# Kernel optimization log

Measured on AMD Instinct MI355X. Metric: run time of the kernel, lower is better.

Reference implementation:

```python
import jax, jax.numpy as jnp
import numpy as np

M_FACTORS = [8, 8, 8, 8]
N_FACTORS = [8, 8, 8, 8]
RANK = 8
E = 8
B = 8
SEQ = 512
M_IN = int(np.prod(M_FACTORS))   # 4096
N_OUT = int(np.prod(N_FACTORS))  # 4096


def setup_inputs() -> dict:
    key = jax.random.key(0)
    k1, k2, k3, k4, k5 = jax.random.split(key, 5)
    X = jax.random.normal(k1, (B, SEQ, M_IN), dtype=jnp.float32)
    gates = jax.random.uniform(k2, (B, E), dtype=jnp.float32)
    # TT cores: [E, r_i, factor, r_{i+1}]; boundary ranks are 1.
    core_first = jax.random.normal(k3, (E, 1, M_FACTORS[0], RANK), dtype=jnp.float32)
    cores_mid = jax.random.normal(k4, (6, E, RANK, 8, RANK), dtype=jnp.float32)
    core_last = jax.random.normal(k5, (E, RANK, N_FACTORS[-1], 1), dtype=jnp.float32)
    return {"X": X, "gates": gates, "core_first": core_first,
            "cores_mid": cores_mid, "core_last": core_last}


def _tt_forward(X, gates, core_first, cores_mid, core_last):
    b, s, _ = X.shape
    # View X as [B, 1, seq, m_k-1, ..., m_0] (m factors reversed), rank dim = 1.
    tt = X.reshape((b, s) + tuple(M_FACTORS[::-1]))[:, None]
    cores = [core_first] + [cores_mid[i] for i in range(cores_mid.shape[0])] + [core_last]
    num_m = len(M_FACTORS)
    # Input-factor contractions: 'b r ... m, b r m p -> b p ...'
    for i in range(num_m):
        merged = jnp.einsum('be,ermp->brmp', gates, cores[i])  # [B, r, m_f, p]
        tt = jnp.einsum('br...m,brmp->bp...', tt, merged)
    # Output-factor expansions: 'b r ..., b r n p -> b p ... n'
    for i in range(len(N_FACTORS)):
        merged = jnp.einsum('be,ernp->brnp', gates, cores[num_m + i])  # [B, r, n_f, p]
        tt = jnp.einsum('br...,brnp->bp...n', tt, merged)
    return tt.reshape(b, s, -1)  # [B, seq, prod(n_factors)]


def reference(X, gates, core_first, cores_mid, core_last):
    return _tt_forward(X, gates, core_first, cores_mid, core_last)
```

## Files before the change

### kernel.cpp

```cpp
#include <hip/hip_runtime.h>


#define MC_ 8

__global__ __launch_bounds__(256) void k_compose(
    const float* __restrict__ gates,
    const float* __restrict__ core_first,
    const float* __restrict__ cores_mid,
    const float* __restrict__ core_last,
    float* __restrict__ Kin,
    float* __restrict__ Kout)
{
  const int part = blockIdx.x;
  const int b    = blockIdx.y;
  const int t    = threadIdx.x;

  __shared__ float g[8];
  __shared__ float mg[3200];
  __shared__ __align__(16) float A2[512];
  __shared__ __align__(16) float A3[4096];
  __shared__ __align__(16) float C2[512];
  __shared__ __align__(16) float C3[4096];

  if (t < 8) g[t] = gates[b*8 + t];
  __syncthreads();

  for (int idx = t; idx < 3200; idx += 256) {
    float acc = 0.f;
    if (idx < 64) {
      #pragma unroll
      for (int e = 0; e < 8; ++e) acc += g[e] * core_first[e*64 + idx];
    } else if (idx < 3136) {
      const int i = (idx - 64) >> 9;
      const int w = (idx - 64) & 511;
      #pragma unroll
      for (int e = 0; e < 8; ++e) acc += g[e] * cores_mid[(i*8 + e)*512 + w];
    } else {
      const int w = idx - 3136;
      #pragma unroll
      for (int e = 0; e < 8; ++e) acc += g[e] * core_last[e*64 + w];
    }
    mg[idx] = acc;
  }
  __syncthreads();

  const float* mg0 = mg;
  const float* mg1 = mg + 64;
  const float* mg2 = mg + 64 + 512;
  const float* mg3 = mg + 64 + 1024;
  const float* mg4 = mg + 64 + 1536;
  const float* mg5 = mg + 64 + 2048;
  const float* mg6 = mg + 64 + 2560;
  const float* mg7 = mg + 3136;

  for (int idx = t; idx < 1024; idx += 256) {
    if (idx < 512) {
      const int mm = idx >> 3, p2 = idx & 7;
      const int m1 = mm >> 3, m0 = mm & 7;
      float acc = 0.f;
      #pragma unroll
      for (int p1 = 0; p1 < 8; ++p1)
        acc += mg0[m0*8 + p1] * mg1[p1*64 + m1*8 + p2];
      A2[idx] = acc;
    } else {
      const int id = idx - 512;
      const int p6 = id >> 6, n2 = (id >> 3) & 7, n3 = id & 7;
      float acc = 0.f;
      #pragma unroll
      for (int p7 = 0; p7 < 8; ++p7)
        acc += mg6[p6*64 + n2*8 + p7] * mg7[p7*8 + n3];
      C2[id] = acc;
    }
  }
  __syncthreads();

  for (int idx = t; idx < 8192; idx += 256) {
    if (idx < 4096) {
      const int rest = idx >> 3, p3 = idx & 7;
      const int m2 = rest >> 6, mm = rest & 63;
      float acc = 0.f;
      #pragma unroll
      for (int p2 = 0; p2 < 8; ++p2)
        acc += A2[mm*8 + p2] * mg2[p2*64 + m2*8 + p3];
      A3[idx] = acc;
    } else {
      const int id = idx - 4096;
      const int p5 = id >> 9, n1 = (id >> 6) & 7, nn = id & 63;
      float acc = 0.f;
      #pragma unroll
      for (int p6 = 0; p6 < 8; ++p6)
        acc += mg5[p5*64 + n1*8 + p6] * C2[p6*64 + nn];
      C3[id] = acc;
    }
  }
  __syncthreads();

  {
    float* kb = Kin + b*32768 + part*4096;
    #pragma unroll
    for (int rr = 0; rr < 2; ++rr) {
      const int r = t*2 + rr;
      #pragma unroll
      for (int p4 = 0; p4 < 8; ++p4) {
        float acc = 0.f;
        #pragma unroll
        for (int p3 = 0; p3 < 8; ++p3)
          acc += A3[r*8 + p3] * mg3[p3*64 + part*8 + p4];
        kb[r*8 + p4] = acc;
      }
    }
    float* ob = Kout + b*32768 + part*512;
    #pragma unroll
    for (int jj = 0; jj < 2; ++jj) {
      const int j = t*2 + jj;
      #pragma unroll
      for (int p4 = 0; p4 < 8; ++p4) {
        float acc = 0.f;
        #pragma unroll
        for (int p5 = 0; p5 < 8; ++p5)
          acc += mg4[p4*64 + part*8 + p5] * C3[p5*512 + j];
        ob[p4*4096 + j] = acc;
      }
    }
  }
}

#define XPAD 516

__global__ __launch_bounds__(256) void k_vpart(
    const float* __restrict__ X,
    const float* __restrict__ Kin,
    float* __restrict__ Vpart)
{
  const int stile = blockIdx.x;
  const int mc    = blockIdx.y;
  const int b     = blockIdx.z;
  const int t     = threadIdx.x;

  __shared__ __align__(16) float xs[16 * XPAD];
  __shared__ __align__(16) float lkT[8 * XPAD];
  __shared__ float vred[2 * 16 * 8];

  {
    const float* xbase = X + ((size_t)(b*512 + stile*16) * 4096) + mc*512;
    #pragma unroll
    for (int i = 0; i < 8; ++i) {
      const int idx = t + i*256;
      const int r = idx >> 7;
      const int c = idx & 127;
      const float4 v = ((const float4*)(xbase + (size_t)r*4096))[c];
      *(float4*)&xs[r*XPAD + c*4] = v;
    }
  }
  {
    const float4* kb = (const float4*)(Kin + b*32768 + mc*4096);
    #pragma unroll
    for (int i = 0; i < 4; ++i) {
      const int idx = t + i*256;
      const int m  = idx >> 1;
      const int ph = (idx & 1) * 4;
      const float4 v = kb[idx];
      lkT[(ph+0)*XPAD + m] = v.x;
      lkT[(ph+1)*XPAD + m] = v.y;
      lkT[(ph+2)*XPAD + m] = v.z;
      lkT[(ph+3)*XPAD + m] = v.w;
    }
  }
  __syncthreads();

  {
    const int h  = t >> 7;
    const int sp = t & 127;
    const int sl = sp >> 3;
    const int p  = sp & 7;
    const float* xrow = &xs[sl*XPAD + h*256];
    const float* krow = &lkT[p*XPAD + h*256];
    float acc = 0.f;
    #pragma unroll 8
    for (int j = 0; j < 64; ++j) {
      const float4 a = *(const float4*)(xrow + j*4);
      const float4 k = *(const float4*)(krow + j*4);
      acc += a.x*k.x + a.y*k.y + a.z*k.z + a.w*k.w;
    }
    vred[t] = acc;
  }
  __syncthreads();

  if (t < 128) {
    const float v = vred[t] + vred[128 + t];
    Vpart[((size_t)(b*MC_ + mc)*512 + stile*16)*8 + t] = v;
  }
}

__global__ __launch_bounds__(256) void k_out(
    const float* __restrict__ Vpart,
    const float* __restrict__ Kout,
    float* __restrict__ Out)
{
  const int nc = blockIdx.x;
  const int sg = blockIdx.y;
  const int b  = blockIdx.z;
  const int t  = threadIdx.x;

  __shared__ __align__(16) float vs[32*8];

  {
    const float* vp = Vpart + ((size_t)b*MC_*512 + sg*32)*8 + t;
    float a = 0.f;
    #pragma unroll
    for (int mc = 0; mc < MC_; ++mc) a += vp[(size_t)mc*512*8];
    vs[t] = a;
  }

  float4 kr[8];
  {
    const float* kb = Kout + b*32768 + nc*1024 + t*4;
    #pragma unroll
    for (int p = 0; p < 8; ++p) kr[p] = *(const float4*)(kb + p*4096);
  }
  __syncthreads();

  float* ob = Out + (size_t)(b*512 + sg*32)*4096 + nc*1024 + t*4;
  for (int s = 0; s < 32; ++s) {
    const float* vv = &vs[s*8];
    float o0 = 0.f, o1 = 0.f, o2 = 0.f, o3 = 0.f;
    #pragma unroll
    for (int p = 0; p < 8; ++p) {
      const float v = vv[p];
      o0 += v * kr[p].x; o1 += v * kr[p].y; o2 += v * kr[p].z; o3 += v * kr[p].w;
    }
    *(float4*)(ob + (size_t)s*4096) = make_float4(o0, o1, o2, o3);
  }
}

extern "C" void kernel_launch(void* const* d_in, const int* in_sizes, int n_in,
                              void* d_out, int out_size, void* d_ws, size_t ws_size,
                              hipStream_t stream) {
  const float* X     = (const float*)d_in[0];
  const float* gates = (const float*)d_in[1];
  const float* cf    = (const float*)d_in[2];
  const float* cm    = (const float*)d_in[3];
  const float* cl    = (const float*)d_in[4];
  float* out = (float*)d_out;

  float* ws    = (float*)d_ws;
  float* Kin   = ws;
  float* Kout  = ws + 262144;
  float* Vpart = ws + 524288;

  k_compose<<<dim3(8, 8),          256, 0, stream>>>(gates, cf, cm, cl, Kin, Kout);
  k_vpart <<<dim3(32, MC_, 8),     256, 0, stream>>>(X, Kin, Vpart);
  k_out   <<<dim3(4, 16, 8),       256, 0, stream>>>(Vpart, Kout, out);
}
```

Before: 137.2 us.

## Fuse input projection and output expansion into one kernel with transposed Kin

Merges the X·Kin reduction and the V·Kout expansion into a single kernel, so the Vpart intermediate and one launch go away. Each block now covers 8 sequence rows across all of M, streaming transposed Kin chunks through shared memory with register prefetch and reducing with wave shuffles. The compose kernel writes Kin transposed and pads A3 to avoid shared-memory bank conflicts. The cost is a smaller grid (512 blocks), higher register use, and each block re-reading the full per-batch Kin and Kout.

```diff
diff --git a/kernel.cpp b/kernel.cpp
--- a/kernel.cpp
+++ b/kernel.cpp
@@ -1,14 +1,12 @@
 #include <hip/hip_runtime.h>
 
-
-#define MC_ 8
 
 __global__ __launch_bounds__(256) void k_compose(
     const float* __restrict__ gates,
     const float* __restrict__ core_first,
     const float* __restrict__ cores_mid,
     const float* __restrict__ core_last,
-    float* __restrict__ Kin,
+    float* __restrict__ KinT,
     float* __restrict__ Kout)
 {
   const int part = blockIdx.x;
@@ -18,7 +16,7 @@
   __shared__ float g[8];
   __shared__ float mg[3200];
   __shared__ __align__(16) float A2[512];
-  __shared__ __align__(16) float A3[4096];
+  __shared__ __align__(16) float A3[512 * 9];
   __shared__ __align__(16) float C2[512];
   __shared__ __align__(16) float C3[4096];
 
@@ -82,7 +80,7 @@
       #pragma unroll
       for (int p2 = 0; p2 < 8; ++p2)
         acc += A2[mm*8 + p2] * mg2[p2*64 + m2*8 + p3];
-      A3[idx] = acc;
+      A3[rest*9 + p3] = acc;
     } else {
       const int id = idx - 4096;
       const int p5 = id >> 9, n1 = (id >> 6) & 7, nn = id & 63;
@@ -96,23 +94,23 @@
   __syncthreads();
 
   {
-    float* kb = Kin + b*32768 + part*4096;
+    float* kb = KinT + b*32768;
     #pragma unroll
     for (int rr = 0; rr < 2; ++rr) {
-      const int r = t*2 + rr;
+      const int r = rr*256 + t;
       #pragma unroll
       for (int p4 = 0; p4 < 8; ++p4) {
         float acc = 0.f;
         #pragma unroll
         for (int p3 = 0; p3 < 8; ++p3)
-          acc += A3[r*8 + p3] * mg3[p3*64 + part*8 + p4];
-        kb[r*8 + p4] = acc;
+          acc += A3[r*9 + p3] * mg3[p3*64 + part*8 + p4];
+        kb[p4*4096 + part*512 + r] = acc;
       }
     }
     float* ob = Kout + b*32768 + part*512;
     #pragma unroll
     for (int jj = 0; jj < 2; ++jj) {
-      const int j = t*2 + jj;
+      const int j = jj*256 + t;
       #pragma unroll
       for (int p4 = 0; p4 < 8; ++p4) {
         float acc = 0.f;
@@ -125,111 +123,124 @@
   }
 }
 
-#define XPAD 516
-
-__global__ __launch_bounds__(256) void k_vpart(
+__global__ __launch_bounds__(256, 2) void k_fused(
     const float* __restrict__ X,
-    const float* __restrict__ Kin,
-    float* __restrict__ Vpart)
-{
-  const int stile = blockIdx.x;
-  const int mc    = blockIdx.y;
-  const int b     = blockIdx.z;
-  const int t     = threadIdx.x;
-
-  __shared__ __align__(16) float xs[16 * XPAD];
-  __shared__ __align__(16) float lkT[8 * XPAD];
-  __shared__ float vred[2 * 16 * 8];
-
-  {
-    const float* xbase = X + ((size_t)(b*512 + stile*16) * 4096) + mc*512;
-    #pragma unroll
-    for (int i = 0; i < 8; ++i) {
-      const int idx = t + i*256;
-      const int r = idx >> 7;
-      const int c = idx & 127;
-      const float4 v = ((const float4*)(xbase + (size_t)r*4096))[c];
-      *(float4*)&xs[r*XPAD + c*4] = v;
-    }
-  }
-  {
-    const float4* kb = (const float4*)(Kin + b*32768 + mc*4096);
-    #pragma unroll
-    for (int i = 0; i < 4; ++i) {
-      const int idx = t + i*256;
-      const int m  = idx >> 1;
-      const int ph = (idx & 1) * 4;
-      const float4 v = kb[idx];
-      lkT[(ph+0)*XPAD + m] = v.x;
-      lkT[(ph+1)*XPAD + m] = v.y;
-      lkT[(ph+2)*XPAD + m] = v.z;
-      lkT[(ph+3)*XPAD + m] = v.w;
-    }
-  }
-  __syncthreads();
-
-  {
-    const int h  = t >> 7;
-    const int sp = t & 127;
-    const int sl = sp >> 3;
-    const int p  = sp & 7;
-    const float* xrow = &xs[sl*XPAD + h*256];
-    const float* krow = &lkT[p*XPAD + h*256];
-    float acc = 0.f;
-    #pragma unroll 8
-    for (int j = 0; j < 64; ++j) {
-      const float4 a = *(const float4*)(xrow + j*4);
-      const float4 k = *(const float4*)(krow + j*4);
-      acc += a.x*k.x + a.y*k.y + a.z*k.z + a.w*k.w;
-    }
-    vred[t] = acc;
-  }
-  __syncthreads();
-
-  if (t < 128) {
-    const float v = vred[t] + vred[128 + t];
-    Vpart[((size_t)(b*MC_ + mc)*512 + stile*16)*8 + t] = v;
-  }
-}
-
-__global__ __launch_bounds__(256) void k_out(
-    const float* __restrict__ Vpart,
+    const float* __restrict__ KinT,
     const float* __restrict__ Kout,
     float* __restrict__ Out)
 {
-  const int nc = blockIdx.x;
-  const int sg = blockIdx.y;
-  const int b  = blockIdx.z;
-  const int t  = threadIdx.x;
-
-  __shared__ __align__(16) float vs[32*8];
+  const int stile = blockIdx.x;
+  const int b     = blockIdx.y;
+  const int t     = threadIdx.x;
+  const int lane  = t & 63;
+  const int sp    = t >> 6;
+
+  __shared__ __align__(16) float lkT[8 * 1024];
+  __shared__ __align__(16) float vs[8 * 8];
+
+  const int s0 = stile * 8;
+
+  const float* ksrc = KinT + (size_t)b*32768 + t*4;
+  float*       kdst = lkT + t*4;
+  float4 R[8];
+
+  float4 acc[2][8];
+  #pragma unroll
+  for (int s2 = 0; s2 < 2; ++s2)
+    #pragma unroll
+    for (int p = 0; p < 8; ++p) acc[s2][p] = make_float4(0.f, 0.f, 0.f, 0.f);
+
+  const float* xb = X + ((size_t)(b*512 + s0 + sp*2)) * 4096 + lane*4;
+
+  #pragma unroll
+  for (int i = 0; i < 8; ++i) R[i] = *(const float4*)(ksrc + i*4096);
+  #pragma unroll
+  for (int i = 0; i < 8; ++i) *(float4*)(kdst + i*1024) = R[i];
+  __syncthreads();
+
+  #pragma unroll
+  for (int mc = 0; mc < 4; ++mc) {
+    if (mc < 3) {
+      #pragma unroll
+      for (int i = 0; i < 8; ++i)
+        R[i] = *(const float4*)(ksrc + i*4096 + (mc + 1)*1024);
+    }
+    #pragma unroll
+    for (int j = 0; j < 4; ++j) {
+      const float4 x0 = *(const float4*)(xb + (mc*256 + j*64)*4);
+      const float4 x1 = *(const float4*)(xb + 4096 + (mc*256 + j*64)*4);
+      #pragma unroll
+      for (int p = 0; p < 8; ++p) {
+        const float4 k = *(const float4*)(lkT + p*1024 + (j*64 + lane)*4);
+        acc[0][p].x += x0.x*k.x; acc[0][p].y += x0.y*k.y;
+        acc[0][p].z += x0.z*k.z; acc[0][p].w += x0.w*k.w;
+        acc[1][p].x += x1.x*k.x; acc[1][p].y += x1.y*k.y;
+        acc[1][p].z += x1.z*k.z; acc[1][p].w += x1.w*k.w;
+      }
+    }
+    __syncthreads();
+    if (mc < 3) {
+      #pragma unroll
+      for (int i = 0; i < 8; ++i) *(float4*)(kdst + i*1024) = R[i];
+      __syncthreads();
+    }
+  }
 
   {
-    const float* vp = Vpart + ((size_t)b*MC_*512 + sg*32)*8 + t;
-    float a = 0.f;
-    #pragma unroll
-    for (int mc = 0; mc < MC_; ++mc) a += vp[(size_t)mc*512*8];
-    vs[t] = a;
-  }
-
-  float4 kr[8];
-  {
-    const float* kb = Kout + b*32768 + nc*1024 + t*4;
-    #pragma unroll
-    for (int p = 0; p < 8; ++p) kr[p] = *(const float4*)(kb + p*4096);
-  }
-  __syncthreads();
-
-  float* ob = Out + (size_t)(b*512 + sg*32)*4096 + nc*1024 + t*4;
-  for (int s = 0; s < 32; ++s) {
-    const float* vv = &vs[s*8];
-    float o0 = 0.f, o1 = 0.f, o2 = 0.f, o3 = 0.f;
-    #pragma unroll
-    for (int p = 0; p < 8; ++p) {
-      const float v = vv[p];
-      o0 += v * kr[p].x; o1 += v * kr[p].y; o2 += v * kr[p].z; o3 += v * kr[p].w;
-    }
-    *(float4*)(ob + (size_t)s*4096) = make_float4(o0, o1, o2, o3);
+    float v[2][8];
+    #pragma unroll
+    for (int s2 = 0; s2 < 2; ++s2) {
+      #pragma unroll
+      for (int p = 0; p < 8; ++p) {
+        float s = acc[s2][p].x + acc[s2][p].y + acc[s2][p].z + acc[s2][p].w;
+        s += __shfl_xor(s, 1);
+        s += __shfl_xor(s, 2);
+        s += __shfl_xor(s, 4);
+        s += __shfl_xor(s, 8);
+        s += __shfl_xor(s, 16);
+        s += __shfl_xor(s, 32);
+        v[s2][p] = s;
+      }
+    }
+    if (lane == 0) {
+      #pragma unroll
+      for (int s2 = 0; s2 < 2; ++s2)
+        #pragma unroll
+        for (int p = 0; p < 8; ++p)
+          vs[(sp*2 + s2)*8 + p] = v[s2][p];
+    }
+  }
+  __syncthreads();
+
+  float4 vA[8], vB[8];
+  #pragma unroll
+  for (int s = 0; s < 8; ++s) {
+    vA[s] = *(const float4*)(vs + s*8);
+    vB[s] = *(const float4*)(vs + s*8 + 4);
+  }
+
+  const float* kob = Kout + (size_t)b*32768 + t*4;
+  float*       ob  = Out + ((size_t)(b*512 + s0))*4096 + t*4;
+
+  #pragma unroll
+  for (int nc = 0; nc < 4; ++nc) {
+    float4 kr[8];
+    #pragma unroll
+    for (int p = 0; p < 8; ++p)
+      kr[p] = *(const float4*)(kob + p*4096 + nc*1024);
+    #pragma unroll
+    for (int s = 0; s < 8; ++s) {
+      float4 o;
+      o.x = vA[s].x*kr[0].x + vA[s].y*kr[1].x + vA[s].z*kr[2].x + vA[s].w*kr[3].x
+          + vB[s].x*kr[4].x + vB[s].y*kr[5].x + vB[s].z*kr[6].x + vB[s].w*kr[7].x;
+      o.y = vA[s].x*kr[0].y + vA[s].y*kr[1].y + vA[s].z*kr[2].y + vA[s].w*kr[3].y
+          + vB[s].x*kr[4].y + vB[s].y*kr[5].y + vB[s].z*kr[6].y + vB[s].w*kr[7].y;
+      o.z = vA[s].x*kr[0].z + vA[s].y*kr[1].z + vA[s].z*kr[2].z + vA[s].w*kr[3].z
+          + vB[s].x*kr[4].z + vB[s].y*kr[5].z + vB[s].z*kr[6].z + vB[s].w*kr[7].z;
+      o.w = vA[s].x*kr[0].w + vA[s].y*kr[1].w + vA[s].z*kr[2].w + vA[s].w*kr[3].w
+          + vB[s].x*kr[4].w + vB[s].y*kr[5].w + vB[s].z*kr[6].w + vB[s].w*kr[7].w;
+      *(float4*)(ob + (size_t)s*4096 + nc*1024) = o;
+    }
   }
 }
 
@@ -243,12 +254,10 @@
   const float* cl    = (const float*)d_in[4];
   float* out = (float*)d_out;
 
-  float* ws    = (float*)d_ws;
-  float* Kin   = ws;
-  float* Kout  = ws + 262144;
-  float* Vpart = ws + 524288;
-
-  k_compose<<<dim3(8, 8),          256, 0, stream>>>(gates, cf, cm, cl, Kin, Kout);
-  k_vpart <<<dim3(32, MC_, 8),     256, 0, stream>>>(X, Kin, Vpart);
-  k_out   <<<dim3(4, 16, 8),       256, 0, stream>>>(Vpart, Kout, out);
+  float* ws   = (float*)d_ws;
+  float* KinT = ws;
+  float* Kout = ws + 262144;
+
+  k_compose<<<dim3(8, 8),  256, 0, stream>>>(gates, cf, cm, cl, KinT, Kout);
+  k_fused <<<dim3(64, 8), 256, 0, stream>>>(X, KinT, Kout, out);
 }
```

After: 171.3 us. 24.8% more time.
